# Performance work log

Hardware: AMD Instinct MI355X
Metric: run time of the kernel (lower is better)

The kernel has to match this reference:

```python
import jax, jax.numpy as jnp
import numpy as np

DIM = 512
HEADS = 8
DH = DIM // HEADS  # 64

def setup_inputs() -> dict:
    key = jax.random.key(0)
    ks = jax.random.split(key, 10)
    s = 1.0 / np.sqrt(DIM)
    return {
        "x": jax.random.normal(ks[0], (8, 4096, DIM), dtype=jnp.float32),
        "x_d": jax.random.normal(ks[1], (8, 4096, DIM), dtype=jnp.float32),
        "W_qkv_rgb": jax.random.normal(ks[2], (DIM, 3 * DIM), dtype=jnp.float32) * s,
        "W_qkv_T": jax.random.normal(ks[3], (DIM, 3 * DIM), dtype=jnp.float32) * s,
        "temperature_rgb": jnp.ones((HEADS, 1, 1), dtype=jnp.float32),
        "temperature_T": jnp.ones((HEADS, 1, 1), dtype=jnp.float32),
        "W_proj_rgb": jax.random.normal(ks[4], (DIM, DIM), dtype=jnp.float32) * s,
        "b_proj_rgb": jnp.zeros((DIM,), dtype=jnp.float32),
        "W_proj_T": jax.random.normal(ks[5], (DIM, DIM), dtype=jnp.float32) * s,
        "b_proj_T": jnp.zeros((DIM,), dtype=jnp.float32),
    }

def _split_qkv(t, W):
    # t: (B,N,C) -> q,k,v each (B,H,d,N)  (channels-as-tokens layout)
    B, N, C = t.shape
    qkv = (t @ W).reshape(B, N, 3, HEADS, DH)
    qkv = qkv.transpose(2, 0, 3, 4, 1)  # (3,B,H,d,N)
    return qkv[0], qkv[1], qkv[2]

def _l2norm(a):
    # normalize over last axis (token dim N), matching F.normalize eps=1e-12
    n = jnp.sqrt(jnp.sum(a * a, axis=-1, keepdims=True))
    return a / jnp.maximum(n, 1e-12)

def _xca(q, k, v, temp):
    # q,k,v: (B,H,d,N); temp: (H,1,1) -> out (B,N,C)
    attn = jnp.einsum("bhdn,bhen->bhde", q, k) * temp  # (B,H,d,d)
    attn = jax.nn.softmax(attn, axis=-1)
    out = jnp.einsum("bhde,bhen->bhdn", attn, v)  # (B,H,d,N)
    B = out.shape[0]
    N = out.shape[-1]
    return out.transpose(0, 3, 1, 2).reshape(B, N, HEADS * DH)

def reference(x, x_d, W_qkv_rgb, W_qkv_T, temperature_rgb, temperature_T,
              W_proj_rgb, b_proj_rgb, W_proj_T, b_proj_T):
    q_rgb, k_rgb, v_rgb = _split_qkv(x, W_qkv_rgb)
    q_T, k_T, v_T = _split_qkv(x_d, W_qkv_T)
    q_rgb = _l2norm(q_rgb); k_rgb = _l2norm(k_rgb)
    q_T = _l2norm(q_T); k_T = _l2norm(k_T)
    out_rgb = _xca(q_rgb, k_T, v_T, temperature_rgb)
    out_T = _xca(q_T, k_rgb, v_rgb, temperature_T)
    out_rgb = out_rgb @ W_proj_rgb + b_proj_rgb
    out_T = out_T @ W_proj_T + b_proj_T
    return out_rgb, out_T
```

## Files before the change

### kernel.cpp

```cpp
#include <hip/hip_runtime.h>
#include <hip/hip_bf16.h>
#include <math.h>
#include <stdint.h>

typedef __bf16 bf16;
typedef __bf16 bf16x8 __attribute__((ext_vector_type(8)));
typedef float  floatx4 __attribute__((ext_vector_type(4)));

#define HEADS 8
#define DH    64
#define NB    8
#define NTOK  4096
#define CDIM  512
#define MTOT  32768
#define PART_STRIDE 16777216L

__device__ __forceinline__ void gload16(const bf16* g, bf16* l) {
    __builtin_amdgcn_global_load_lds(
        (const __attribute__((address_space(1))) unsigned int*)g,
        (__attribute__((address_space(3))) unsigned int*)l,
        16, 0, 0);
}

__global__ void detect_kernel(const bf16* __restrict__ w, int* __restrict__ flag)
{
    __shared__ int cnt[256];
    int c = 0;
    for (int i = 0; i < 64; ++i) {
        float v = fabsf((float)w[threadIdx.x + i * 256]);
        if (v > 1e3f) c++;
    }
    cnt[threadIdx.x] = c;
    __syncthreads();
    if (threadIdx.x == 0) {
        int s = 0;
        for (int i = 0; i < 256; ++i) s += cnt[i];
        *flag = (s > 500) ? 1 : 0;
    }
}

__global__ void misc_kernel(const void* t0, const void* t1, const void* b0, const void* b1,
                            const int* __restrict__ flag, float* __restrict__ misc)
{
    bool f32 = (*flag != 0);
    int tid = threadIdx.x;
    #define RD(p, i) (f32 ? ((const float*)(p))[i] : (float)((const bf16*)(p))[i])
    if (tid < 8) { misc[tid] = RD(t0, tid); misc[8 + tid] = RD(t1, tid); }
    for (int i = tid; i < 512; i += 256) {
        misc[16 + i]  = RD(b0, i);
        misc[528 + i] = RD(b1, i);
    }
    #undef RD
}

__global__ void wt_kernel(const void* __restrict__ W, bf16* __restrict__ Wt, int K, int N,
                          const int* __restrict__ flag)
{
    int idx = blockIdx.x * 256 + threadIdx.x;
    if (idx >= K * N) return;
    bool f32 = (*flag != 0);
    int n = idx / K;
    int k = idx - n * K;
    float v = f32 ? ((const float*)W)[k * N + n] : (float)((const bf16*)W)[k * N + n];
    Wt[idx] = (bf16)v;
}

__global__ void cast_kernel(const void* __restrict__ X, bf16* __restrict__ Y,
                            const int* __restrict__ flag)
{
    size_t i = ((size_t)blockIdx.x * 256 + threadIdx.x) * 8;
    if (*flag) {
        const float* xf = (const float*)X + i;
        float4 a = *(const float4*)xf;
        float4 b = *(const float4*)(xf + 4);
        bf16 t[8] = {(bf16)a.x, (bf16)a.y, (bf16)a.z, (bf16)a.w,
                     (bf16)b.x, (bf16)b.y, (bf16)b.z, (bf16)b.w};
        *(uint4*)(Y + i) = *(uint4*)t;
    } else {
        *(uint4*)(Y + i) = *(const uint4*)((const bf16*)X + i);
    }
}

__global__ __launch_bounds__(512, 2) void gemm_bt(
    const bf16* __restrict__ A, const bf16* __restrict__ Bt,
    const float* __restrict__ bias, void* __restrict__ C, bf16* __restrict__ Cv,
    long c_base, const int* __restrict__ cflag)
{
    __shared__ bf16 lds[2][2][2][128 * 64];

    const int tid  = threadIdx.x;
    const int lane = tid & 63;
    const int w    = tid >> 6;
    const int wmi  = w >> 2;
    const int wni  = w & 3;
    const int l15  = lane & 15;
    const int quad = lane >> 4;

    const int m0 = blockIdx.x * 256;
    const int n0 = blockIdx.y * 256;

    const int rl0 = w * 16 + (lane >> 3);
    const int swz = ((lane & 7) ^ (rl0 & 7)) * 8;
    const bf16* Abase = A  + (size_t)(m0 + rl0) * 512 + swz;
    const bf16* Bbase = Bt + (size_t)(n0 + rl0) * 512 + swz;
    const int ldst0 = w * 1024;

    const int rxor  = l15 & 7;
    const int k0off = (quad ^ rxor) * 8;
    const int k1off = ((4 + quad) ^ rxor) * 8;
    const bf16* Ah0 = &lds[0][0][wmi][l15 * 64];
    const bf16* Ah1 = &lds[1][0][wmi][l15 * 64];
    const bf16* Bh0 = &lds[0][1][wni >> 1][((wni & 1) * 64 + l15) * 64];
    const bf16* Bh1 = &lds[1][1][wni >> 1][((wni & 1) * 64 + l15) * 64];

    bf16x8 aR[4][2], bR[4][2];
    floatx4 acc[8][4] = {};

#define STAGE_A(b, h, t) do { \
    const bf16* _g = Abase + (h) * 65536 + (t) * 64; \
    gload16(_g,        &lds[b][0][h][ldst0]); \
    gload16(_g + 4096, &lds[b][0][h][ldst0 + 512]); \
} while (0)
#define STAGE_B(b, h, t) do { \
    const bf16* _g = Bbase + (h) * 65536 + (t) * 64; \
    gload16(_g,        &lds[b][1][h][ldst0]); \
    gload16(_g + 4096, &lds[b][1][h][ldst0 + 512]); \
} while (0)
#define RD_A(b, qm) do { \
    _Pragma("unroll") for (int _i = 0; _i < 4; ++_i) { \
        aR[_i][0] = *(const bf16x8*)(Ah##b + ((qm) * 4 + _i) * 1024 + k0off); \
        aR[_i][1] = *(const bf16x8*)(Ah##b + ((qm) * 4 + _i) * 1024 + k1off); \
    } \
} while (0)
#define RD_B(b, qn) do { \
    _Pragma("unroll") for (int _j = 0; _j < 2; ++_j) { \
        bR[(qn) * 2 + _j][0] = *(const bf16x8*)(Bh##b + ((qn) * 2 + _j) * 1024 + k0off); \
        bR[(qn) * 2 + _j][1] = *(const bf16x8*)(Bh##b + ((qn) * 2 + _j) * 1024 + k1off); \
    } \
} while (0)
#define MM(qm, qn) do { \
    _Pragma("unroll") for (int _i = 0; _i < 4; ++_i) \
    _Pragma("unroll") for (int _j = 0; _j < 2; ++_j) { \
        acc[(qm)*4+_i][(qn)*2+_j] = __builtin_amdgcn_mfma_f32_16x16x32_bf16( \
            aR[_i][0], bR[(qn)*2+_j][0], acc[(qm)*4+_i][(qn)*2+_j], 0, 0, 0); \
        acc[(qm)*4+_i][(qn)*2+_j] = __builtin_amdgcn_mfma_f32_16x16x32_bf16( \
            aR[_i][1], bR[(qn)*2+_j][1], acc[(qm)*4+_i][(qn)*2+_j], 0, 0, 0); \
    } \
} while (0)
#define SYNC   asm volatile("s_barrier" ::: "memory")
#define VMW(n) asm volatile("s_waitcnt vmcnt(" #n ")" ::: "memory")
#define PRIO1  __builtin_amdgcn_s_setprio(1)
#define PRIO0  __builtin_amdgcn_s_setprio(0)

#define TILE(t, b, nb, W) do { \
     \
    RD_A(b, 0); RD_B(b, 0); \
    if ((t) + 1 < 8) STAGE_B(nb, 1, (t) + 1); \
    SYNC; PRIO1; MM(0, 0); PRIO0; SYNC; \
     \
    RD_B(b, 1); \
    if ((t) + 1 < 8) STAGE_A(nb, 1, (t) + 1); \
    SYNC; PRIO1; MM(0, 1); PRIO0; SYNC; \
     \
    RD_A(b, 1); \
    if ((t) + 2 < 8) STAGE_B(b, 0, (t) + 2); \
    SYNC; PRIO1; MM(1, 1); PRIO0; SYNC; \
     \
    if ((t) + 2 < 8) STAGE_A(b, 0, (t) + 2); \
    SYNC; PRIO1; MM(1, 0); PRIO0; \
    VMW(W); SYNC; \
} while (0)

    STAGE_A(0, 0, 0); STAGE_A(0, 1, 0); STAGE_B(0, 0, 0); STAGE_B(0, 1, 0);
    STAGE_B(1, 0, 1); STAGE_A(1, 0, 1);
    VMW(4);
    SYNC;

    TILE(0, 0, 1, 4);
    TILE(1, 1, 0, 4);
    TILE(2, 0, 1, 4);
    TILE(3, 1, 0, 4);
    TILE(4, 0, 1, 4);
    TILE(5, 1, 0, 4);
    TILE(6, 0, 1, 0);
    TILE(7, 1, 0, 0);

#undef TILE
#undef STAGE_A
#undef STAGE_B
#undef RD_A
#undef RD_B
#undef MM
#undef SYNC
#undef VMW
#undef PRIO1
#undef PRIO0

    const bool cf32 = cflag && (*cflag != 0);
    const int  part = n0 >> 9;
    const long rowB = (long)m0 + wmi * 128 + quad * 4;
    const int  colB = (n0 & 511) + wni * 64 + l15;

    float bv[4];
    #pragma unroll
    for (int fj = 0; fj < 4; ++fj)
        bv[fj] = bias ? bias[n0 + wni * 64 + fj * 16 + l15] : 0.0f;

    if (part == 2) {
        #pragma unroll
        for (int fi = 0; fi < 8; ++fi)
            #pragma unroll
            for (int rr = 0; rr < 4; ++rr) {
                bf16* op = Cv + (rowB + fi * 16 + rr) * CDIM + colB;
                #pragma unroll
                for (int fj = 0; fj < 4; ++fj)
                    op[fj * 16] = (bf16)acc[fi][fj][rr];
            }
    } else if (cf32) {
        float* Cp = (float*)C + c_base + (long)part * PART_STRIDE;
        #pragma unroll
        for (int fi = 0; fi < 8; ++fi)
            #pragma unroll
            for (int rr = 0; rr < 4; ++rr) {
                float* op = Cp + (rowB + fi * 16 + rr) * CDIM + colB;
                #pragma unroll
                for (int fj = 0; fj < 4; ++fj)
                    op[fj * 16] = acc[fi][fj][rr] + bv[fj];
            }
    } else {
        bf16* Cp = (bf16*)C + c_base + (long)part * PART_STRIDE;
        #pragma unroll
        for (int fi = 0; fi < 8; ++fi)
            #pragma unroll
            for (int rr = 0; rr < 4; ++rr) {
                bf16* op = Cp + (rowB + fi * 16 + rr) * CDIM + colB;
                #pragma unroll
                for (int fj = 0; fj < 4; ++fj)
                    op[fj * 16] = (bf16)(acc[fi][fj][rr] + bv[fj]);
            }
    }
}

__device__ inline void unpack8(uint4 u, float* dst) {
    uint32_t w[4] = {u.x, u.y, u.z, u.w};
    #pragma unroll
    for (int i = 0; i < 4; ++i) {
        dst[2 * i]     = __uint_as_float(w[i] << 16);
        dst[2 * i + 1] = __uint_as_float(w[i] & 0xffff0000u);
    }
}

__global__ __launch_bounds__(256) void xca_gk(
    const bf16* __restrict__ Q0, const bf16* __restrict__ K0,
    const bf16* __restrict__ Q1, const bf16* __restrict__ K1,
    float* __restrict__ G, float* __restrict__ NQ, float* __restrict__ NK)
{
    __shared__ float qc[64][68];
    __shared__ float kc[64][68];

    int bid = blockIdx.x;
    int nq4 = bid & 3;
    int h   = (bid >> 2) & 7;
    int b   = (bid >> 5) & 7;
    int s   = bid >> 8;
    int sbh = s * 64 + b * 8 + h;

    const bf16* qsrc = s ? Q1 : Q0;
    const bf16* ksrc = s ? K0 : K1;

    int tid  = threadIdx.x;
    int nloc = tid >> 2;
    int d8   = (tid & 3) * 8;
    int d0   = (tid >> 4) * 4;
    int e0   = (tid & 15) * 4;

    float acc[4][4] = {};
    float nacc = 0.f;

    int n_start = nq4 * 1024;
    for (int ch = 0; ch < 16; ++ch) {
        int ng = n_start + ch * 64 + nloc;
        const bf16* qp = qsrc + (long)(b * NTOK + ng) * CDIM + h * DH;
        const bf16* kp = ksrc + (long)(b * NTOK + ng) * CDIM + h * DH;
        uint4 qA = *(const uint4*)(qp + d8);
        uint4 qB = *(const uint4*)(qp + 32 + d8);
        uint4 kA = *(const uint4*)(kp + d8);
        uint4 kB = *(const uint4*)(kp + 32 + d8);
        __syncthreads();
        unpack8(qA, &qc[nloc][d8]);
        unpack8(qB, &qc[nloc][32 + d8]);
        unpack8(kA, &kc[nloc][d8]);
        unpack8(kB, &kc[nloc][32 + d8]);
        __syncthreads();

        if (tid < 64) {
            #pragma unroll 8
            for (int n = 0; n < 64; ++n) { float v = qc[n][tid]; nacc += v * v; }
        } else if (tid < 128) {
            int dd = tid - 64;
            #pragma unroll 8
            for (int n = 0; n < 64; ++n) { float v = kc[n][dd]; nacc += v * v; }
        }
        #pragma unroll 4
        for (int n = 0; n < 64; ++n) {
            floatx4 qd = *(floatx4*)&qc[n][d0];
            floatx4 ke = *(floatx4*)&kc[n][e0];
            #pragma unroll
            for (int i = 0; i < 4; ++i)
                #pragma unroll
                for (int j = 0; j < 4; ++j)
                    acc[i][j] += qd[i] * ke[j];
        }
    }
    float* Gp = G + (sbh * 64 + d0) * 64 + e0;
    #pragma unroll
    for (int i = 0; i < 4; ++i)
        #pragma unroll
        for (int j = 0; j < 4; ++j)
            atomicAdd(&Gp[i * 64 + j], acc[i][j]);
    if (tid < 64)       atomicAdd(&NQ[sbh * 64 + tid], nacc);
    else if (tid < 128) atomicAdd(&NK[sbh * 64 + tid - 64], nacc);
}

__global__ void xca_soft(const float* __restrict__ G,
                         const float* __restrict__ NQ, const float* __restrict__ NK,
                         const float* __restrict__ misc, bf16* __restrict__ P)
{
    int sbh = blockIdx.x;
    int s = sbh >> 6;
    int h = sbh & 7;
    int d = threadIdx.x;

    __shared__ float rk[64];
    rk[d] = 1.0f / fmaxf(sqrtf(NK[sbh * 64 + d]), 1e-12f);
    __syncthreads();

    float rq = 1.0f / fmaxf(sqrtf(NQ[sbh * 64 + d]), 1e-12f);
    float t  = misc[s * 8 + h];
    const float* Gr = G + (sbh * 64 + d) * 64;

    float a[64];
    float mx = -1e30f;
    #pragma unroll
    for (int e = 0; e < 64; ++e) {
        a[e] = Gr[e] * rq * rk[e] * t;
        mx = fmaxf(mx, a[e]);
    }
    float sum = 0.f;
    #pragma unroll
    for (int e = 0; e < 64; ++e) { a[e] = expf(a[e] - mx); sum += a[e]; }
    float inv = 1.0f / sum;
    bf16* Pr = P + (sbh * 64 + d) * 64;
    #pragma unroll
    for (int e = 0; e < 64; ++e) Pr[e] = (bf16)(a[e] * inv);
}

__global__ __launch_bounds__(256) void xca_pv(
    const bf16* __restrict__ V0, const bf16* __restrict__ V1,
    const bf16* __restrict__ P, bf16* __restrict__ xca)
{
    int bid = blockIdx.x;
    int nq4 = bid & 3;
    int h   = (bid >> 2) & 7;
    int b   = (bid >> 5) & 7;
    int s   = bid >> 8;
    int sbh = s * 64 + b * 8 + h;

    const bf16* vsrc = s ? V0 : V1;

    int tid = threadIdx.x;
    int lane = tid & 63;
    int wave = tid >> 6;
    int l15 = lane & 15;
    int quad = lane >> 4;

    const bf16* Pb = P + sbh * 4096;
    bf16x8 pf[4][2];
    #pragma unroll
    for (int i = 0; i < 4; ++i)
        #pragma unroll
        for (int h2 = 0; h2 < 2; ++h2)
            pf[i][h2] = *(const bf16x8*)&Pb[(i * 16 + l15) * 64 + h2 * 32 + quad * 8];

    int n_start = nq4 * 1024 + wave * 256;
    for (int nt = 0; nt < 16; ++nt) {
        int nb = n_start + nt * 16;
        const bf16* vp = vsrc + (long)(b * NTOK + nb + l15) * CDIM + h * DH + quad * 8;
        bf16x8 v0 = *(const bf16x8*)vp;
        bf16x8 v1 = *(const bf16x8*)(vp + 32);
        floatx4 acc[4] = {};
        #pragma unroll
        for (int i = 0; i < 4; ++i) {
            acc[i] = __builtin_amdgcn_mfma_f32_16x16x32_bf16(v0, pf[i][0], acc[i], 0, 0, 0);
            acc[i] = __builtin_amdgcn_mfma_f32_16x16x32_bf16(v1, pf[i][1], acc[i], 0, 0, 0);
        }
        bf16* op = xca + (long)((s * NB + b) * NTOK + nb + quad * 4) * CDIM + h * DH + l15;
        #pragma unroll
        for (int i = 0; i < 4; ++i)
            #pragma unroll
            for (int r = 0; r < 4; ++r)
                op[(long)r * CDIM + i * 16] = (bf16)acc[i][r];
    }
}

extern "C" void kernel_launch(void* const* d_in, const int* in_sizes, int n_in,
                              void* d_out, int out_size, void* d_ws, size_t ws_size,
                              hipStream_t stream)
{
    const void* x     = d_in[0];
    const void* x_d   = d_in[1];
    const void* Wq0   = d_in[2];
    const void* Wq1   = d_in[3];
    const void* temp0 = d_in[4];
    const void* temp1 = d_in[5];
    const void* Wp0   = d_in[6];
    const void* bp0   = d_in[7];
    const void* Wp1   = d_in[8];
    const void* bp1   = d_in[9];

    char* ws = (char*)d_ws;
    bf16*  Q0   = (bf16*)(ws);
    bf16*  K0   = (bf16*)(ws + 33554432);
    bf16*  Q1   = (bf16*)(ws + 67108864);
    bf16*  K1   = (bf16*)(ws + 100663296);
    bf16*  Xb0  = (bf16*)(ws + 134217728);
    bf16*  Xb1  = (bf16*)(ws + 167772160);
    bf16*  xca  = (bf16*)(ws + 134217728);
    bf16*  wtq0 = (bf16*)(ws + 201326592);
    bf16*  wtq1 = (bf16*)(ws + 202899456);
    bf16*  wtp0 = (bf16*)(ws + 204472320);
    bf16*  wtp1 = (bf16*)(ws + 204996608);
    float* G    = (float*)(ws + 205520896);
    float* NQ   = (float*)(ws + 207618048);
    float* NK   = (float*)(ws + 207650816);
    bf16*  P    = (bf16*)(ws + 207683584);
    int*   flag = (int*)(ws + 208732160);
    float* misc = (float*)(ws + 208732224);

    bf16* V0 = (bf16*)d_out;
    bf16* V1 = (bf16*)d_out + PART_STRIDE;

    hipMemsetAsync(ws + 205520896, 0, 2162688, stream);

    detect_kernel<<<1, 256, 0, stream>>>((const bf16*)Wq0, flag);
    misc_kernel<<<1, 256, 0, stream>>>(temp0, temp1, bp0, bp1, flag, misc);

    wt_kernel<<<(512 * 1536 + 255) / 256, 256, 0, stream>>>(Wq0, wtq0, 512, 1536, flag);
    wt_kernel<<<(512 * 1536 + 255) / 256, 256, 0, stream>>>(Wq1, wtq1, 512, 1536, flag);
    wt_kernel<<<(512 * 512 + 255) / 256, 256, 0, stream>>>(Wp0, wtp0, 512, 512, flag);
    wt_kernel<<<(512 * 512 + 255) / 256, 256, 0, stream>>>(Wp1, wtp1, 512, 512, flag);

    cast_kernel<<<8192, 256, 0, stream>>>(x,   Xb0, flag);
    cast_kernel<<<8192, 256, 0, stream>>>(x_d, Xb1, flag);

    gemm_bt<<<dim3(128, 6), 512, 0, stream>>>(Xb0, wtq0, nullptr, Q0, V0, 0L, nullptr);
    gemm_bt<<<dim3(128, 6), 512, 0, stream>>>(Xb1, wtq1, nullptr, Q1, V1, 0L, nullptr);

    xca_gk<<<512, 256, 0, stream>>>(Q0, K0, Q1, K1, G, NQ, NK);
    xca_soft<<<128, 64, 0, stream>>>(G, NQ, NK, misc, P);
    xca_pv<<<512, 256, 0, stream>>>(V0, V1, P, xca);

    gemm_bt<<<dim3(128, 2), 512, 0, stream>>>(xca,               wtp0, misc + 16,  d_out, nullptr, 0L,          flag);
    gemm_bt<<<dim3(128, 2), 512, 0, stream>>>(xca + PART_STRIDE, wtp1, misc + 528, d_out, nullptr, PART_STRIDE, flag);
}
```

Measured before the change: 587.5 us.

## Compute XCA Gram matrix and norms with bf16 MFMA in xca_gk

Replaces the scalar fp32 outer-product loop in xca_gk with bf16 MFMA 16x16x32 instructions on transposed, XOR-swizzled bf16 tiles in shared memory. Squared norms come from the diagonals of the extra MFMA products Q·Q and K·K instead of a separate serial loop over a quarter of the threads. Global loads for the next chunk are issued as register prefetches while the current chunk is being computed. This cuts LDS footprint and ALU work, but adds redundant MFMA work for the norms and more complex indexing.

```diff
diff --git a/kernel.cpp b/kernel.cpp
--- a/kernel.cpp
+++ b/kernel.cpp
@@ -241,22 +241,13 @@
     }
 }
 
-__device__ inline void unpack8(uint4 u, float* dst) {
-    uint32_t w[4] = {u.x, u.y, u.z, u.w};
-    #pragma unroll
-    for (int i = 0; i < 4; ++i) {
-        dst[2 * i]     = __uint_as_float(w[i] << 16);
-        dst[2 * i + 1] = __uint_as_float(w[i] & 0xffff0000u);
-    }
-}
-
 __global__ __launch_bounds__(256) void xca_gk(
     const bf16* __restrict__ Q0, const bf16* __restrict__ K0,
     const bf16* __restrict__ Q1, const bf16* __restrict__ K1,
     float* __restrict__ G, float* __restrict__ NQ, float* __restrict__ NK)
 {
-    __shared__ float qc[64][68];
-    __shared__ float kc[64][68];
+    __shared__ bf16 Tq[64 * 72];
+    __shared__ bf16 Tk[64 * 72];
 
     int bid = blockIdx.x;
     int nq4 = bid & 3;
@@ -269,57 +260,108 @@
     const bf16* ksrc = s ? K0 : K1;
 
     int tid  = threadIdx.x;
-    int nloc = tid >> 2;
-    int d8   = (tid & 3) * 8;
-    int d0   = (tid >> 4) * 4;
-    int e0   = (tid & 15) * 4;
-
-    float acc[4][4] = {};
-    float nacc = 0.f;
-
-    int n_start = nq4 * 1024;
-    for (int ch = 0; ch < 16; ++ch) {
-        int ng = n_start + ch * 64 + nloc;
-        const bf16* qp = qsrc + (long)(b * NTOK + ng) * CDIM + h * DH;
-        const bf16* kp = ksrc + (long)(b * NTOK + ng) * CDIM + h * DH;
-        uint4 qA = *(const uint4*)(qp + d8);
-        uint4 qB = *(const uint4*)(qp + 32 + d8);
-        uint4 kA = *(const uint4*)(kp + d8);
-        uint4 kB = *(const uint4*)(kp + 32 + d8);
+    int lane = tid & 63;
+    int wv   = tid >> 6;
+    int wr   = wv >> 1;
+    int wc   = wv & 1;
+    int l15  = lane & 15;
+    int quad = lane >> 4;
+    bool isQ = (wv == 0 || wv == 3);
+
+    int m_thr = tid & 7;
+    int d0    = m_thr * 8;
+    int u     = tid >> 3;
+    int u_w   = u ^ (m_thr << 2);
+    int wbase = d0 * 72 + 2 * u_w;
+
+    int aoff[2][2], boff[2][2];
+    #pragma unroll
+    for (int i = 0; i < 2; ++i) {
+        int ra = wr * 32 + i * 16 + l15;
+        int rb = wc * 32 + i * 16 + l15;
+        #pragma unroll
+        for (int ss = 0; ss < 2; ++ss) {
+            int ulog = ss * 16 + quad * 4;
+            aoff[i][ss] = ra * 72 + 2 * (ulog ^ ((ra >> 3) << 2));
+            boff[i][ss] = rb * 72 + 2 * (ulog ^ ((rb >> 3) << 2));
+        }
+    }
+
+    long gbase = (long)(b * NTOK + nq4 * 1024) * CDIM + h * DH + d0;
+    const bf16* qg = qsrc + gbase;
+    const bf16* kg = ksrc + gbase;
+
+    floatx4 accG[2][2] = {};
+    floatx4 accN[2] = {};
+
+    uint4 qA, qB, kA, kB;
+    {
+        size_t off = (size_t)(2 * u) * CDIM;
+        qA = *(const uint4*)(qg + off);
+        qB = *(const uint4*)(qg + off + CDIM);
+        kA = *(const uint4*)(kg + off);
+        kB = *(const uint4*)(kg + off + CDIM);
+    }
+
+    for (int t = 0; t < 16; ++t) {
         __syncthreads();
-        unpack8(qA, &qc[nloc][d8]);
-        unpack8(qB, &qc[nloc][32 + d8]);
-        unpack8(kA, &kc[nloc][d8]);
-        unpack8(kB, &kc[nloc][32 + d8]);
+        {
+            const unsigned short* pa = (const unsigned short*)&qA;
+            const unsigned short* pb = (const unsigned short*)&qB;
+            const unsigned short* pc = (const unsigned short*)&kA;
+            const unsigned short* pd = (const unsigned short*)&kB;
+            #pragma unroll
+            for (int j = 0; j < 8; ++j) {
+                *(uint32_t*)((char*)Tq + (size_t)(wbase + j * 72) * 2) =
+                    (uint32_t)pa[j] | ((uint32_t)pb[j] << 16);
+                *(uint32_t*)((char*)Tk + (size_t)(wbase + j * 72) * 2) =
+                    (uint32_t)pc[j] | ((uint32_t)pd[j] << 16);
+            }
+        }
         __syncthreads();
-
-        if (tid < 64) {
-            #pragma unroll 8
-            for (int n = 0; n < 64; ++n) { float v = qc[n][tid]; nacc += v * v; }
-        } else if (tid < 128) {
-            int dd = tid - 64;
-            #pragma unroll 8
-            for (int n = 0; n < 64; ++n) { float v = kc[n][dd]; nacc += v * v; }
+        if (t + 1 < 16) {
+            size_t off = (size_t)((t + 1) * 64 + 2 * u) * CDIM;
+            qA = *(const uint4*)(qg + off);
+            qB = *(const uint4*)(qg + off + CDIM);
+            kA = *(const uint4*)(kg + off);
+            kB = *(const uint4*)(kg + off + CDIM);
         }
-        #pragma unroll 4
-        for (int n = 0; n < 64; ++n) {
-            floatx4 qd = *(floatx4*)&qc[n][d0];
-            floatx4 ke = *(floatx4*)&kc[n][e0];
+        #pragma unroll
+        for (int ss = 0; ss < 2; ++ss) {
+            bf16x8 a0 = *(const bf16x8*)&Tq[aoff[0][ss]];
+            bf16x8 a1 = *(const bf16x8*)&Tq[aoff[1][ss]];
+            bf16x8 b0 = *(const bf16x8*)&Tk[boff[0][ss]];
+            bf16x8 b1 = *(const bf16x8*)&Tk[boff[1][ss]];
+            accG[0][0] = __builtin_amdgcn_mfma_f32_16x16x32_bf16(a0, b0, accG[0][0], 0, 0, 0);
+            accG[0][1] = __builtin_amdgcn_mfma_f32_16x16x32_bf16(a0, b1, accG[0][1], 0, 0, 0);
+            accG[1][0] = __builtin_amdgcn_mfma_f32_16x16x32_bf16(a1, b0, accG[1][0], 0, 0, 0);
+            accG[1][1] = __builtin_amdgcn_mfma_f32_16x16x32_bf16(a1, b1, accG[1][1], 0, 0, 0);
+            if (isQ) {
+                accN[0] = __builtin_amdgcn_mfma_f32_16x16x32_bf16(a0, a0, accN[0], 0, 0, 0);
+                accN[1] = __builtin_amdgcn_mfma_f32_16x16x32_bf16(a1, a1, accN[1], 0, 0, 0);
+            } else {
+                accN[0] = __builtin_amdgcn_mfma_f32_16x16x32_bf16(b0, b0, accN[0], 0, 0, 0);
+                accN[1] = __builtin_amdgcn_mfma_f32_16x16x32_bf16(b1, b1, accN[1], 0, 0, 0);
+            }
+        }
+    }
+
+    float* Gp = G + (size_t)sbh * 4096;
+    #pragma unroll
+    for (int i = 0; i < 2; ++i)
+        #pragma unroll
+        for (int j = 0; j < 2; ++j)
             #pragma unroll
-            for (int i = 0; i < 4; ++i)
-                #pragma unroll
-                for (int j = 0; j < 4; ++j)
-                    acc[i][j] += qd[i] * ke[j];
-        }
-    }
-    float* Gp = G + (sbh * 64 + d0) * 64 + e0;
-    #pragma unroll
-    for (int i = 0; i < 4; ++i)
-        #pragma unroll
-        for (int j = 0; j < 4; ++j)
-            atomicAdd(&Gp[i * 64 + j], acc[i][j]);
-    if (tid < 64)       atomicAdd(&NQ[sbh * 64 + tid], nacc);
-    else if (tid < 128) atomicAdd(&NK[sbh * 64 + tid - 64], nacc);
+            for (int rr = 0; rr < 4; ++rr)
+                atomicAdd(&Gp[(wr * 32 + i * 16 + quad * 4 + rr) * 64 + wc * 32 + j * 16 + l15],
+                          accG[i][j][rr]);
+
+    float* Np  = isQ ? NQ : NK;
+    int nbase  = (isQ ? wr : wc) * 32;
+    if ((l15 >> 2) == quad) {
+        atomicAdd(&Np[(size_t)sbh * 64 + nbase + l15],      accN[0][l15 & 3]);
+        atomicAdd(&Np[(size_t)sbh * 64 + nbase + 16 + l15], accN[1][l15 & 3]);
+    }
 }
 
 __global__ void xca_soft(const float* __restrict__ G,
```

New measurement: 528.9 us. 10.0% less time.
